# Performance work log

Measured on AMD Instinct MI355X. Metric: run time of the kernel, lower is better.

The kernel has to match this reference:

```python
import jax, jax.numpy as jnp
import numpy as np
from jax import lax

# Key identity used: modulating ALL weights of output channel o by s_o (with no bias
# inside the modulated conv, as in the source where F.conv2d(..., bias=None)) is
# mathematically identical to a plain conv followed by per-(batch, out_channel)
# scaling of the output. This collapses the per-sample Python loop into one conv.

def _upsample2x(x):
    # nearest-neighbor x2, matching F.interpolate(scale_factor=2) default mode
    return jnp.repeat(jnp.repeat(x, 2, axis=2), 2, axis=3)

def _conv(x, w):
    return lax.conv_general_dilated(
        x, w, window_strides=(1, 1), padding=[(1, 1), (1, 1)],
        dimension_numbers=("NCHW", "OIHW", "NCHW"))

def _modconv(x, style, w, fc_w, fc_b):
    # style_fc: [B, style_dim] -> [B, out_ch]
    s = style @ fc_w.T + fc_b          # [B, O]
    y = _conv(x, w)                    # [B, O, H, W]
    return y * s[:, :, None, None]


def setup_inputs() -> dict:
    key = jax.random.key(0)
    ks = jax.random.split(key, 16)
    B, SD = 8, 512
    chans = [(512, 256), (256, 128), (128, 64), (64, 64), (64, 64)]
    inp = {
        "x": jax.random.normal(ks[0], (B, 512, 8, 8), jnp.float32),
        "style": jax.random.normal(ks[1], (B, SD), jnp.float32),
    }
    for i, (ci, co) in enumerate(chans, start=1):
        inp[f"w{i}"] = jax.random.normal(ks[2 * i], (co, ci, 3, 3), jnp.float32) * (1.0 / np.sqrt(ci * 9))
        inp[f"fw{i}"] = jax.random.normal(ks[2 * i + 1], (co, SD), jnp.float32) * (1.0 / np.sqrt(SD))
        inp[f"fb{i}"] = jnp.ones((co,), jnp.float32)
    inp["wf"] = jax.random.normal(ks[12], (3, 64, 3, 3), jnp.float32) * (1.0 / np.sqrt(64 * 9))
    inp["bf"] = jnp.zeros((3,), jnp.float32)
    return inp


def reference(x, style, w1, fw1, fb1, w2, fw2, fb2, w3, fw3, fb3,
              w4, fw4, fb4, w5, fw5, fb5, wf, bf):
    x = _upsample2x(x)
    x = jax.nn.relu(_modconv(x, style, w1, fw1, fb1))
    x = _upsample2x(x)
    x = jax.nn.relu(_modconv(x, style, w2, fw2, fb2))
    x = _upsample2x(x)
    x = jax.nn.relu(_modconv(x, style, w3, fw3, fb3))
    x = _upsample2x(x)
    x = jax.nn.relu(_modconv(x, style, w4, fw4, fb4))
    x = _upsample2x(x)
    x = jax.nn.relu(_modconv(x, style, w5, fw5, fb5))
    x = _conv(x, wf) + bf[None, :, None, None]
    return x
```

## Files before the change

kernel.cpp:

```cpp
#include <hip/hip_runtime.h>
#include <hip/hip_bf16.h>
#include <cstddef>

typedef __bf16 bf16x8 __attribute__((ext_vector_type(8)));
typedef float f32x4 __attribute__((ext_vector_type(4)));


__global__ void convert_x_kernel(const float* __restrict__ x, __hip_bfloat16* __restrict__ act0) {
    int t = blockIdx.x * 256 + threadIdx.x;
    int c = t & 511; int rest = t >> 9;
    int w = rest & 7; rest >>= 3; int h = rest & 7; int b = rest >> 3;
    act0[t] = __float2bfloat16(x[((b * 512 + c) * 8 + h) * 8 + w]);
}

__global__ void wtrans_all_kernel(const float* __restrict__ w1, __hip_bfloat16* __restrict__ o1,
                                  const float* __restrict__ w2, __hip_bfloat16* __restrict__ o2,
                                  const float* __restrict__ w3, __hip_bfloat16* __restrict__ o3,
                                  const float* __restrict__ w4, __hip_bfloat16* __restrict__ o4,
                                  const float* __restrict__ w5, __hip_bfloat16* __restrict__ o5,
                                  const float* __restrict__ wf, __hip_bfloat16* __restrict__ of) {
    int t = blockIdx.x * 256 + threadIdx.x;
    if (t >= 1631232) return;
    if (t < 1548288) {
        const float* w; __hip_bfloat16* o; int lgci, lgco;
        if      (t < 1179648) { w = w1; o = o1; lgci = 9; lgco = 8; }
        else if (t < 1474560) { t -= 1179648; w = w2; o = o2; lgci = 8; lgco = 7; }
        else                  { t -= 1474560; w = w3; o = o3; lgci = 7; lgco = 6; }
        int CI = 1 << lgci;
        int ci = t & (CI - 1);
        int co = (t >> lgci) & ((1 << lgco) - 1);
        int tap = t >> (lgci + lgco);
        o[t] = __float2bfloat16(w[((size_t)co * CI + ci) * 9 + tap]);
    } else if (t < 1622016) {
        const float* w; __hip_bfloat16* o;
        if (t < 1585152) { t -= 1548288; w = w4; o = o4; }
        else             { t -= 1585152; w = w5; o = o5; }
        int j  = t & 7;
        int ln = (t >> 3) & 63;
        int ch = (t >> 9) & 1;
        int nt = (t >> 10) & 3;
        int tap = t >> 12;
        int rr = ln & 15, qq = ln >> 4;
        int co = nt * 16 + rr;
        int ci = ch * 32 + qq * 8 + j;
        o[t] = __float2bfloat16(w[((size_t)co * 64 + ci) * 9 + tap]);
    } else {
        int u = t - 1622016;
        int j  = u & 7;
        int ln = (u >> 3) & 63;
        int ch = (u >> 9) & 1;
        int tap = u >> 10;
        int rr = ln & 15, qq = ln >> 4;
        int ci = ch * 32 + qq * 8 + j;
        float v = (rr < 3) ? wf[((size_t)rr * 64 + ci) * 9 + tap] : 0.f;
        of[u] = __float2bfloat16(v);
    }
}

__global__ void style_all_kernel(const float* __restrict__ style,
                                 const float* __restrict__ fw1, const float* __restrict__ fb1,
                                 const float* __restrict__ fw2, const float* __restrict__ fb2,
                                 const float* __restrict__ fw3, const float* __restrict__ fb3,
                                 const float* __restrict__ fw4, const float* __restrict__ fb4,
                                 const float* __restrict__ fw5, const float* __restrict__ fb5,
                                 float* __restrict__ S) {
    int wvid = blockIdx.x * 4 + (threadIdx.x >> 6);
    int lane = threadIdx.x & 63;
    const float* fw; const float* fb; int lg, sOff, local;
    if      (wvid < 2048) { fw = fw1; fb = fb1; lg = 8; sOff = 0;    local = wvid; }
    else if (wvid < 3072) { fw = fw2; fb = fb2; lg = 7; sOff = 2048; local = wvid - 2048; }
    else if (wvid < 3584) { fw = fw3; fb = fb3; lg = 6; sOff = 3072; local = wvid - 3072; }
    else if (wvid < 4096) { fw = fw4; fb = fb4; lg = 6; sOff = 3584; local = wvid - 3584; }
    else                  { fw = fw5; fb = fb5; lg = 6; sOff = 4096; local = wvid - 4096; }
    int b = local >> lg, o = local & ((1 << lg) - 1);
    const float* sb = style + b * 512;
    const float* fwo = fw + (size_t)o * 512;
    float p = 0.f;
    #pragma unroll
    for (int k = lane; k < 512; k += 64) p += sb[k] * fwo[k];
    #pragma unroll
    for (int off = 32; off > 0; off >>= 1) p += __shfl_down(p, off);
    if (lane == 0) S[sOff + local] = p + fb[o];
}

template <int CI, int CO, int HS, int WS>
__launch_bounds__(256)
__global__ void conv_partial_kernel(const __hip_bfloat16* __restrict__ actIn,
                                    const __hip_bfloat16* __restrict__ wtr,
                                    float* __restrict__ Part) {
    constexpr int HO = HS * 2, WO = WS * 2;
    constexpr size_t sliceN = (size_t)8 * HO * WO * CO;
    const int tid = threadIdx.x;
    const int lane = tid & 63, wv = tid >> 6;
    const int r = lane & 15, q = lane >> 4;
    const int pw = WO / 16, ppb = (HO / 16) * pw;
    const int b = blockIdx.x / ppb;
    const int prest = blockIdx.x - b * ppb;
    const int ph = prest / pw, pwi = prest - ph * pw;
    const int oh0 = ph * 16, ow0 = pwi * 16;
    const int sh0 = oh0 >> 1, sw0 = ow0 >> 1;
    const int n0 = blockIdx.y * 64;
    const int ciOff = blockIdx.z * 64;

    __shared__ alignas(16) __hip_bfloat16 Tile[100 * 72];
    __shared__ alignas(16) __hip_bfloat16 Wlds[2][64 * 72];

    f32x4 acc[4][4];
    #pragma unroll
    for (int i = 0; i < 4; ++i)
        #pragma unroll
        for (int j = 0; j < 4; ++j) acc[i][j] = f32x4{0.f, 0.f, 0.f, 0.f};

    for (int i = tid; i < 800; i += 256) {
        int pix = i >> 3, koct = i & 7;
        int tr = pix / 10, tc2 = pix - tr * 10;
        int su = sh0 - 1 + tr, sv = sw0 - 1 + tc2;
        uint4 v = {0, 0, 0, 0};
        if (su >= 0 && su < HS && sv >= 0 && sv < WS)
            v = *(const uint4*)(actIn + ((size_t)((b * HS + su) * WS + sv) * CI + ciOff + koct * 8));
        *(uint4*)&Tile[pix * 72 + koct * 8] = v;
    }
    for (int i = tid; i < 512; i += 256) {
        int co = i >> 3, koct = i & 7;
        *(uint4*)&Wlds[0][co * 72 + koct * 8] =
            *(const uint4*)(wtr + ((size_t)(n0 + co)) * CI + ciOff + koct * 8);
    }
    __syncthreads();

    #pragma unroll 1
    for (int tap = 0; tap < 9; ++tap) {
        const bool pf = (tap < 8);
        uint4 wr0 = {0,0,0,0}, wr1 = {0,0,0,0};
        if (pf) {
            int co0 = tid >> 3, k0 = tid & 7;
            wr0 = *(const uint4*)(wtr + ((size_t)(tap + 1) * CO + n0 + co0) * CI + ciOff + k0 * 8);
            int i1 = tid + 256; int co1 = i1 >> 3, k1 = i1 & 7;
            wr1 = *(const uint4*)(wtr + ((size_t)(tap + 1) * CO + n0 + co1) * CI + ciOff + k1 * 8);
        }
        const int dyv = tap / 3;
        const int dxm1 = tap - dyv * 3 - 1;
        const int tc = ((r + dxm1) >> 1) + 1;
        int apix[4];
        #pragma unroll
        for (int mt = 0; mt < 4; ++mt)
            apix[mt] = ((((wv * 4 + mt) + dyv - 1) >> 1) + 1) * 10 + tc;

        const int buf = tap & 1;
        #pragma unroll
        for (int ch = 0; ch < 2; ++ch) {
            bf16x8 af[4], bfr[4];
            #pragma unroll
            for (int mt = 0; mt < 4; ++mt)
                af[mt] = *(const bf16x8*)&Tile[apix[mt] * 72 + ch * 32 + q * 8];
            #pragma unroll
            for (int nt = 0; nt < 4; ++nt)
                bfr[nt] = *(const bf16x8*)&Wlds[buf][(nt * 16 + r) * 72 + ch * 32 + q * 8];
            #pragma unroll
            for (int mt = 0; mt < 4; ++mt)
                #pragma unroll
                for (int nt = 0; nt < 4; ++nt)
                    acc[mt][nt] = __builtin_amdgcn_mfma_f32_16x16x32_bf16(
                        af[mt], bfr[nt], acc[mt][nt], 0, 0, 0);
        }
        if (pf) {
            int nb = buf ^ 1;
            { int co0 = tid >> 3, k0 = tid & 7;
              *(uint4*)&Wlds[nb][co0 * 72 + k0 * 8] = wr0; }
            { int i1 = tid + 256; int co1 = i1 >> 3, k1 = i1 & 7;
              *(uint4*)&Wlds[nb][co1 * 72 + k1 * 8] = wr1; }
            __syncthreads();
        }
    }

    float* P = Part + (size_t)blockIdx.z * sliceN;
    #pragma unroll
    for (int mt = 0; mt < 4; ++mt) {
        const int prow = wv * 4 + mt;
        #pragma unroll
        for (int t2 = 0; t2 < 4; ++t2) {
            const int pcol = q * 4 + t2;
            const size_t obase = ((size_t)(b * HO + oh0 + prow) * WO + ow0 + pcol) * CO + n0;
            #pragma unroll
            for (int nt = 0; nt < 4; ++nt)
                P[obase + nt * 16 + r] = acc[mt][nt][t2];
        }
    }
}

template <int KS, int CO, int HW>
__launch_bounds__(256)
__global__ void reduce_kernel(const float* __restrict__ Part, const float* __restrict__ S,
                              __hip_bfloat16* __restrict__ actOut) {
    constexpr size_t sliceN = (size_t)8 * HW * CO;
    size_t e = ((size_t)blockIdx.x * 256 + threadIdx.x) * 4;
    if (e >= sliceN) return;
    f32x4 sum = {0.f, 0.f, 0.f, 0.f};
    #pragma unroll
    for (int k = 0; k < KS; ++k) sum += *(const f32x4*)(Part + (size_t)k * sliceN + e);
    const int co = (int)(e & (CO - 1));
    const int b = (int)(e / ((size_t)HW * CO));
    const float* Sb = S + b * CO + co;
    union { ushort4 u; __hip_bfloat16 h[4]; } pack;
    #pragma unroll
    for (int j = 0; j < 4; ++j)
        pack.h[j] = __float2bfloat16(fmaxf(sum[j] * Sb[j], 0.f));
    *(ushort4*)((unsigned short*)actOut + e) = pack.u;
}

template <int HS, int WS>
__launch_bounds__(256)
__global__ void conv_patch_kernel(const __hip_bfloat16* __restrict__ actIn,
                                  const __hip_bfloat16* __restrict__ wpk,
                                  const float* __restrict__ S,
                                  __hip_bfloat16* __restrict__ actOut) {
    constexpr int HO = HS * 2, WO = WS * 2;

    const int tid = threadIdx.x;
    const int lane = tid & 63, wv = tid >> 6;
    const int r = lane & 15, q = lane >> 4;
    const int lane8 = lane * 8;

    const int pw = WO / 16, ppb = (HO / 16) * pw;
    const int b = blockIdx.x / ppb;
    const int prest = blockIdx.x - b * ppb;
    const int ph = prest / pw, pwi = prest - ph * pw;
    const int oh0 = ph * 16, ow0 = pwi * 16;
    const int sh0 = oh0 >> 1, sw0 = ow0 >> 1;

    __shared__ alignas(16) __hip_bfloat16 Tile[100 * 72];

    f32x4 acc[4][4];
    #pragma unroll
    for (int i = 0; i < 4; ++i)
        #pragma unroll
        for (int j = 0; j < 4; ++j) acc[i][j] = f32x4{0.f, 0.f, 0.f, 0.f};

    const int wv4 = wv * 4;

    for (int i = tid; i < 800; i += 256) {
        int pix = i >> 3, koct = i & 7;
        int tr = pix / 10, tc2 = pix - tr * 10;
        int su = sh0 - 1 + tr, sv = sw0 - 1 + tc2;
        uint4 v = {0, 0, 0, 0};
        if (su >= 0 && su < HS && sv >= 0 && sv < WS)
            v = *(const uint4*)(actIn + ((size_t)((b * HS + su) * WS + sv) * 64 + koct * 8));
        *(uint4*)&Tile[pix * 72 + koct * 8] = v;
    }
    __syncthreads();

    bf16x8 bA[4][2], bB[4][2];

    auto loadB = [&](bf16x8 (&dst)[4][2], int tap) {
        #pragma unroll
        for (int nt = 0; nt < 4; ++nt)
            #pragma unroll
            for (int ch = 0; ch < 2; ++ch)
                dst[nt][ch] = *(const bf16x8*)(wpk + ((tap * 8 + nt * 2 + ch) << 9) + lane8);
    };

    auto compute = [&](int tap, bf16x8 (&bfr)[4][2]) {
        const int dyv = tap / 3;
        const int dxm1 = tap - dyv * 3 - 1;
        const int tc = ((r + dxm1) >> 1) + 1;
        int apix[4];
        #pragma unroll
        for (int mt = 0; mt < 4; ++mt)
            apix[mt] = ((((wv4 + mt) + dyv - 1) >> 1) + 1) * 10 + tc;
        #pragma unroll
        for (int ch = 0; ch < 2; ++ch) {
            bf16x8 af[4];
            #pragma unroll
            for (int mt = 0; mt < 4; ++mt)
                af[mt] = *(const bf16x8*)&Tile[apix[mt] * 72 + ch * 32 + q * 8];
            #pragma unroll
            for (int mt = 0; mt < 4; ++mt)
                #pragma unroll
                for (int nt = 0; nt < 4; ++nt)
                    acc[mt][nt] = __builtin_amdgcn_mfma_f32_16x16x32_bf16(
                        af[mt], bfr[nt][ch], acc[mt][nt], 0, 0, 0);
        }
    };

    loadB(bA, 0);
    #pragma unroll 1
    for (int it = 0; it < 4; ++it) {
        loadB(bB, 2 * it + 1);
        compute(2 * it, bA);
        loadB(bA, 2 * it + 2);
        compute(2 * it + 1, bB);
    }
    compute(8, bA);

    float sv_[4];
    #pragma unroll
    for (int nt = 0; nt < 4; ++nt) sv_[nt] = S[b * 64 + nt * 16 + r];
    #pragma unroll
    for (int mt = 0; mt < 4; ++mt) {
        const int prow = wv4 + mt;
        #pragma unroll
        for (int t2 = 0; t2 < 4; ++t2) {
            const int pcol = q * 4 + t2;
            const size_t obase = ((size_t)(b * HO + oh0 + prow) * WO + ow0 + pcol) * 64;
            #pragma unroll
            for (int nt = 0; nt < 4; ++nt)
                actOut[obase + nt * 16 + r] =
                    __float2bfloat16(fmaxf(acc[mt][nt][t2] * sv_[nt], 0.f));
        }
    }
}

__launch_bounds__(256)
__global__ void conv_final_kernel(const __hip_bfloat16* __restrict__ actIn,
                                  const __hip_bfloat16* __restrict__ wpkF,
                                  const float* __restrict__ bias,
                                  float* __restrict__ out) {
    constexpr int HO = 256, WO = 256;
    const int tid = threadIdx.x, lane = tid & 63, wv = tid >> 6;
    const int r = lane & 15, q = lane >> 4;
    const int lane8 = lane * 8;

    const int ppb = 32 * 16;
    const int b = blockIdx.x / ppb;
    const int prest = blockIdx.x - b * ppb;
    const int ph = prest >> 4, pwi = prest & 15;
    const int oh0 = ph * 8, ow0 = pwi * 16;

    __shared__ alignas(16) __hip_bfloat16 Tile[10 * 18 * 72];

    for (int i = tid; i < 1440; i += 256) {
        int pix = i >> 3, koct = i & 7;
        int tr = pix / 18, tc2 = pix - tr * 18;
        int u = oh0 - 1 + tr, v = ow0 - 1 + tc2;
        uint4 val = {0, 0, 0, 0};
        if (u >= 0 && u < HO && v >= 0 && v < WO)
            val = *(const uint4*)(actIn + ((size_t)((b * HO + u) * WO + v) * 64 + koct * 8));
        *(uint4*)&Tile[pix * 72 + koct * 8] = val;
    }
    __syncthreads();

    f32x4 acc[2];
    acc[0] = f32x4{0.f, 0.f, 0.f, 0.f};
    acc[1] = f32x4{0.f, 0.f, 0.f, 0.f};

    #pragma unroll 1
    for (int tap = 0; tap < 9; ++tap) {
        const int dyv = tap / 3;
        const int dxv = tap - dyv * 3;
        const int tc = r + dxv;
        int apix[2];
        #pragma unroll
        for (int mt = 0; mt < 2; ++mt)
            apix[mt] = (wv * 2 + mt + dyv) * 18 + tc;
        #pragma unroll
        for (int ch = 0; ch < 2; ++ch) {
            bf16x8 bfr = *(const bf16x8*)(wpkF + ((tap * 2 + ch) << 9) + lane8);
            #pragma unroll
            for (int mt = 0; mt < 2; ++mt) {
                bf16x8 af = *(const bf16x8*)&Tile[apix[mt] * 72 + ch * 32 + q * 8];
                acc[mt] = __builtin_amdgcn_mfma_f32_16x16x32_bf16(af, bfr, acc[mt], 0, 0, 0);
            }
        }
    }

    if (r < 3) {
        const float bs = bias[r];
        #pragma unroll
        for (int mt = 0; mt < 2; ++mt) {
            const int prow = wv * 2 + mt;
            #pragma unroll
            for (int t2 = 0; t2 < 4; ++t2) {
                const int pcol = q * 4 + t2;
                out[((size_t)(b * 3 + r) << 16) + (oh0 + prow) * 256 + ow0 + pcol] =
                    acc[mt][t2] + bs;
            }
        }
    }
}

extern "C" void kernel_launch(void* const* d_in, const int* in_sizes, int n_in,
                              void* d_out, int out_size, void* d_ws, size_t ws_size,
                              hipStream_t stream) {
    const float* x    = (const float*)d_in[0];
    const float* sty  = (const float*)d_in[1];
    const float* w1   = (const float*)d_in[2];
    const float* fw1  = (const float*)d_in[3];
    const float* fb1  = (const float*)d_in[4];
    const float* w2   = (const float*)d_in[5];
    const float* fw2  = (const float*)d_in[6];
    const float* fb2  = (const float*)d_in[7];
    const float* w3   = (const float*)d_in[8];
    const float* fw3  = (const float*)d_in[9];
    const float* fb3  = (const float*)d_in[10];
    const float* w4   = (const float*)d_in[11];
    const float* fw4  = (const float*)d_in[12];
    const float* fb4  = (const float*)d_in[13];
    const float* w5   = (const float*)d_in[14];
    const float* fw5  = (const float*)d_in[15];
    const float* fb5  = (const float*)d_in[16];
    const float* wf   = (const float*)d_in[17];
    const float* bf   = (const float*)d_in[18];
    float* out = (float*)d_out;

    char* ws = (char*)d_ws;
    size_t off = 0;
    auto alloc = [&](size_t bytes) {
        char* p = ws + off;
        off += (bytes + 255) & ~(size_t)255;
        return p;
    };
    float* S1 = (float*)alloc(8 * 256 * 4);
    float* S2 = (float*)alloc(8 * 128 * 4);
    float* S3 = (float*)alloc(8 * 64 * 4);
    float* S4 = (float*)alloc(8 * 64 * 4);
    float* S5 = (float*)alloc(8 * 64 * 4);
    __hip_bfloat16* act0 = (__hip_bfloat16*)alloc((size_t)262144 * 2);
    __hip_bfloat16* act1 = (__hip_bfloat16*)alloc((size_t)524288 * 2);
    __hip_bfloat16* act2 = (__hip_bfloat16*)alloc((size_t)1048576 * 2);
    __hip_bfloat16* act3 = (__hip_bfloat16*)alloc((size_t)2097152 * 2);
    __hip_bfloat16* act4 = (__hip_bfloat16*)alloc((size_t)8388608 * 2);
    __hip_bfloat16* act5 = (__hip_bfloat16*)alloc((size_t)33554432 * 2);
    __hip_bfloat16* wt1  = (__hip_bfloat16*)alloc((size_t)9 * 256 * 512 * 2);
    __hip_bfloat16* wt2  = (__hip_bfloat16*)alloc((size_t)9 * 128 * 256 * 2);
    __hip_bfloat16* wt3  = (__hip_bfloat16*)alloc((size_t)9 * 64 * 128 * 2);
    __hip_bfloat16* wt4  = (__hip_bfloat16*)alloc((size_t)9 * 64 * 64 * 2);
    __hip_bfloat16* wt5  = (__hip_bfloat16*)alloc((size_t)9 * 64 * 64 * 2);
    __hip_bfloat16* wtF  = (__hip_bfloat16*)alloc((size_t)9 * 16 * 64 * 2);
    if (off > ws_size) return;

    float* Part = (float*)act5;

    convert_x_kernel<<<1024, 256, 0, stream>>>(x, act0);
    wtrans_all_kernel<<<6372, 256, 0, stream>>>(w1, wt1, w2, wt2, w3, wt3,
                                                w4, wt4, w5, wt5, wf, wtF);
    style_all_kernel<<<1152, 256, 0, stream>>>(sty, fw1, fb1, fw2, fb2, fw3, fb3,
                                               fw4, fb4, fw5, fb5, S1);

    conv_partial_kernel<512, 256, 8, 8><<<dim3(8, 4, 8), 256, 0, stream>>>(act0, wt1, Part);
    reduce_kernel<8, 256, 256><<<512, 256, 0, stream>>>(Part, S1, act1);
    conv_partial_kernel<256, 128, 16, 16><<<dim3(32, 2, 4), 256, 0, stream>>>(act1, wt2, Part);
    reduce_kernel<4, 128, 1024><<<1024, 256, 0, stream>>>(Part, S2, act2);
    conv_partial_kernel<128, 64, 32, 32><<<dim3(128, 1, 2), 256, 0, stream>>>(act2, wt3, Part);
    reduce_kernel<2, 64, 4096><<<2048, 256, 0, stream>>>(Part, S3, act3);

    conv_patch_kernel<64, 64><<<dim3(512), 256, 0, stream>>>(act3, wt4, S4, act4);
    conv_patch_kernel<128, 128><<<dim3(2048), 256, 0, stream>>>(act4, wt5, S5, act5);
    conv_final_kernel<<<4096, 256, 0, stream>>>(act5, wtF, bf, out);
}
```

Before: 228.4 us.

## Use 32x32x16 MFMA in patch conv and 512-thread blocks in partial convs

The 64-channel patch conv kernels now use 32x32x16 bf16 MFMA with a 2x2 accumulator tile instead of 16x16x32 with 4x4, and the packed weight layout for layers 4 and 5 is reordered to match the new B-fragment lane mapping. The early split-K partial conv kernels switch from 256 to 512 threads per block, so each wave handles two pixel rows instead of four and the weight staging takes one load per thread. The aim is fewer MFMA issues and fewer LDS fragment reads in the dominant layers, plus more waves to hide latency in the small early layers. In exchange the epilogue uses a more scattered output index pattern, and larger blocks may reduce how many blocks fit per CU.

```diff
diff --git a/kernel.cpp b/kernel.cpp
--- a/kernel.cpp
+++ b/kernel.cpp
@@ -4,6 +4,7 @@
 
 typedef __bf16 bf16x8 __attribute__((ext_vector_type(8)));
 typedef float f32x4 __attribute__((ext_vector_type(4)));
+typedef float f32x16 __attribute__((ext_vector_type(16)));
 
 
 __global__ void convert_x_kernel(const float* __restrict__ x, __hip_bfloat16* __restrict__ act0) {
@@ -37,12 +38,11 @@
         else             { t -= 1585152; w = w5; o = o5; }
         int j  = t & 7;
         int ln = (t >> 3) & 63;
-        int ch = (t >> 9) & 1;
-        int nt = (t >> 10) & 3;
+        int nt = (t >> 9) & 1;
+        int ks = (t >> 10) & 3;
         int tap = t >> 12;
-        int rr = ln & 15, qq = ln >> 4;
-        int co = nt * 16 + rr;
-        int ci = ch * 32 + qq * 8 + j;
+        int co = nt * 32 + (ln & 31);
+        int ci = ks * 16 + (ln >> 5) * 8 + j;
         o[t] = __float2bfloat16(w[((size_t)co * 64 + ci) * 9 + tap]);
     } else {
         int u = t - 1622016;
@@ -84,7 +84,7 @@
 }
 
 template <int CI, int CO, int HS, int WS>
-__launch_bounds__(256)
+__launch_bounds__(512)
 __global__ void conv_partial_kernel(const __hip_bfloat16* __restrict__ actIn,
                                     const __hip_bfloat16* __restrict__ wtr,
                                     float* __restrict__ Part) {
@@ -105,13 +105,13 @@
     __shared__ alignas(16) __hip_bfloat16 Tile[100 * 72];
     __shared__ alignas(16) __hip_bfloat16 Wlds[2][64 * 72];
 
-    f32x4 acc[4][4];
-    #pragma unroll
-    for (int i = 0; i < 4; ++i)
+    f32x4 acc[2][4];
+    #pragma unroll
+    for (int i = 0; i < 2; ++i)
         #pragma unroll
         for (int j = 0; j < 4; ++j) acc[i][j] = f32x4{0.f, 0.f, 0.f, 0.f};
 
-    for (int i = tid; i < 800; i += 256) {
+    for (int i = tid; i < 800; i += 512) {
         int pix = i >> 3, koct = i & 7;
         int tr = pix / 10, tc2 = pix - tr * 10;
         int su = sh0 - 1 + tr, sv = sw0 - 1 + tc2;
@@ -120,8 +120,8 @@
             v = *(const uint4*)(actIn + ((size_t)((b * HS + su) * WS + sv) * CI + ciOff + koct * 8));
         *(uint4*)&Tile[pix * 72 + koct * 8] = v;
     }
-    for (int i = tid; i < 512; i += 256) {
-        int co = i >> 3, koct = i & 7;
+    {
+        int co = tid >> 3, koct = tid & 7;
         *(uint4*)&Wlds[0][co * 72 + koct * 8] =
             *(const uint4*)(wtr + ((size_t)(n0 + co)) * CI + ciOff + koct * 8);
     }
@@ -130,33 +130,31 @@
     #pragma unroll 1
     for (int tap = 0; tap < 9; ++tap) {
         const bool pf = (tap < 8);
-        uint4 wr0 = {0,0,0,0}, wr1 = {0,0,0,0};
+        uint4 wr0 = {0,0,0,0};
         if (pf) {
             int co0 = tid >> 3, k0 = tid & 7;
             wr0 = *(const uint4*)(wtr + ((size_t)(tap + 1) * CO + n0 + co0) * CI + ciOff + k0 * 8);
-            int i1 = tid + 256; int co1 = i1 >> 3, k1 = i1 & 7;
-            wr1 = *(const uint4*)(wtr + ((size_t)(tap + 1) * CO + n0 + co1) * CI + ciOff + k1 * 8);
         }
         const int dyv = tap / 3;
         const int dxm1 = tap - dyv * 3 - 1;
         const int tc = ((r + dxm1) >> 1) + 1;
-        int apix[4];
-        #pragma unroll
-        for (int mt = 0; mt < 4; ++mt)
-            apix[mt] = ((((wv * 4 + mt) + dyv - 1) >> 1) + 1) * 10 + tc;
+        int apix[2];
+        #pragma unroll
+        for (int mt = 0; mt < 2; ++mt)
+            apix[mt] = ((((wv * 2 + mt) + dyv - 1) >> 1) + 1) * 10 + tc;
 
         const int buf = tap & 1;
         #pragma unroll
         for (int ch = 0; ch < 2; ++ch) {
-            bf16x8 af[4], bfr[4];
-            #pragma unroll
-            for (int mt = 0; mt < 4; ++mt)
+            bf16x8 af[2], bfr[4];
+            #pragma unroll
+            for (int mt = 0; mt < 2; ++mt)
                 af[mt] = *(const bf16x8*)&Tile[apix[mt] * 72 + ch * 32 + q * 8];
             #pragma unroll
             for (int nt = 0; nt < 4; ++nt)
                 bfr[nt] = *(const bf16x8*)&Wlds[buf][(nt * 16 + r) * 72 + ch * 32 + q * 8];
             #pragma unroll
-            for (int mt = 0; mt < 4; ++mt)
+            for (int mt = 0; mt < 2; ++mt)
                 #pragma unroll
                 for (int nt = 0; nt < 4; ++nt)
                     acc[mt][nt] = __builtin_amdgcn_mfma_f32_16x16x32_bf16(
@@ -164,18 +162,16 @@
         }
         if (pf) {
             int nb = buf ^ 1;
-            { int co0 = tid >> 3, k0 = tid & 7;
-              *(uint4*)&Wlds[nb][co0 * 72 + k0 * 8] = wr0; }
-            { int i1 = tid + 256; int co1 = i1 >> 3, k1 = i1 & 7;
-              *(uint4*)&Wlds[nb][co1 * 72 + k1 * 8] = wr1; }
+            int co0 = tid >> 3, k0 = tid & 7;
+            *(uint4*)&Wlds[nb][co0 * 72 + k0 * 8] = wr0;
             __syncthreads();
         }
     }
 
     float* P = Part + (size_t)blockIdx.z * sliceN;
     #pragma unroll
-    for (int mt = 0; mt < 4; ++mt) {
-        const int prow = wv * 4 + mt;
+    for (int mt = 0; mt < 2; ++mt) {
+        const int prow = wv * 2 + mt;
         #pragma unroll
         for (int t2 = 0; t2 < 4; ++t2) {
             const int pcol = q * 4 + t2;
@@ -217,7 +213,10 @@
 
     const int tid = threadIdx.x;
     const int lane = tid & 63, wv = tid >> 6;
-    const int r = lane & 15, q = lane >> 4;
+    const int r32 = lane & 31;
+    const int ko  = lane >> 5;
+    const int pcol = r32 & 15;
+    const int rsub = r32 >> 4;
     const int lane8 = lane * 8;
 
     const int pw = WO / 16, ppb = (HO / 16) * pw;
@@ -229,11 +228,13 @@
 
     __shared__ alignas(16) __hip_bfloat16 Tile[100 * 72];
 
-    f32x4 acc[4][4];
-    #pragma unroll
-    for (int i = 0; i < 4; ++i)
-        #pragma unroll
-        for (int j = 0; j < 4; ++j) acc[i][j] = f32x4{0.f, 0.f, 0.f, 0.f};
+    f32x16 acc[2][2];
+    #pragma unroll
+    for (int i = 0; i < 2; ++i)
+        #pragma unroll
+        for (int j = 0; j < 2; ++j)
+            #pragma unroll
+            for (int k = 0; k < 16; ++k) acc[i][j][k] = 0.f;
 
     const int wv4 = wv * 4;
 
@@ -252,32 +253,34 @@
 
     auto loadB = [&](bf16x8 (&dst)[4][2], int tap) {
         #pragma unroll
-        for (int nt = 0; nt < 4; ++nt)
-            #pragma unroll
-            for (int ch = 0; ch < 2; ++ch)
-                dst[nt][ch] = *(const bf16x8*)(wpk + ((tap * 8 + nt * 2 + ch) << 9) + lane8);
+        for (int ks = 0; ks < 4; ++ks)
+            #pragma unroll
+            for (int nt = 0; nt < 2; ++nt)
+                dst[ks][nt] = *(const bf16x8*)(wpk + (((tap * 4 + ks) * 2 + nt) << 9) + lane8);
     };
 
     auto compute = [&](int tap, bf16x8 (&bfr)[4][2]) {
         const int dyv = tap / 3;
         const int dxm1 = tap - dyv * 3 - 1;
-        const int tc = ((r + dxm1) >> 1) + 1;
-        int apix[4];
-        #pragma unroll
-        for (int mt = 0; mt < 4; ++mt)
-            apix[mt] = ((((wv4 + mt) + dyv - 1) >> 1) + 1) * 10 + tc;
-        #pragma unroll
-        for (int ch = 0; ch < 2; ++ch) {
-            bf16x8 af[4];
-            #pragma unroll
-            for (int mt = 0; mt < 4; ++mt)
-                af[mt] = *(const bf16x8*)&Tile[apix[mt] * 72 + ch * 32 + q * 8];
-            #pragma unroll
-            for (int mt = 0; mt < 4; ++mt)
+        const int tc = ((pcol + dxm1) >> 1) + 1;
+        int apix[2];
+        #pragma unroll
+        for (int mt = 0; mt < 2; ++mt) {
+            const int prow = wv4 + mt * 2 + rsub;
+            apix[mt] = (((prow + dyv - 1) >> 1) + 1) * 10 + tc;
+        }
+        #pragma unroll
+        for (int ks = 0; ks < 4; ++ks) {
+            bf16x8 af[2];
+            #pragma unroll
+            for (int mt = 0; mt < 2; ++mt)
+                af[mt] = *(const bf16x8*)&Tile[apix[mt] * 72 + ks * 16 + ko * 8];
+            #pragma unroll
+            for (int mt = 0; mt < 2; ++mt)
                 #pragma unroll
-                for (int nt = 0; nt < 4; ++nt)
-                    acc[mt][nt] = __builtin_amdgcn_mfma_f32_16x16x32_bf16(
-                        af[mt], bfr[nt][ch], acc[mt][nt], 0, 0, 0);
+                for (int nt = 0; nt < 2; ++nt)
+                    acc[mt][nt] = __builtin_amdgcn_mfma_f32_32x32x16_bf16(
+                        af[mt], bfr[ks][nt], acc[mt][nt], 0, 0, 0);
         }
     };
 
@@ -291,20 +294,22 @@
     }
     compute(8, bA);
 
-    float sv_[4];
-    #pragma unroll
-    for (int nt = 0; nt < 4; ++nt) sv_[nt] = S[b * 64 + nt * 16 + r];
-    #pragma unroll
-    for (int mt = 0; mt < 4; ++mt) {
-        const int prow = wv4 + mt;
-        #pragma unroll
-        for (int t2 = 0; t2 < 4; ++t2) {
-            const int pcol = q * 4 + t2;
-            const size_t obase = ((size_t)(b * HO + oh0 + prow) * WO + ow0 + pcol) * 64;
-            #pragma unroll
-            for (int nt = 0; nt < 4; ++nt)
-                actOut[obase + nt * 16 + r] =
-                    __float2bfloat16(fmaxf(acc[mt][nt][t2] * sv_[nt], 0.f));
+    float sv_[2];
+    #pragma unroll
+    for (int nt = 0; nt < 2; ++nt) sv_[nt] = S[b * 64 + nt * 32 + r32];
+    #pragma unroll
+    for (int mt = 0; mt < 2; ++mt) {
+        #pragma unroll
+        for (int nt = 0; nt < 2; ++nt) {
+            const int co = nt * 32 + r32;
+            #pragma unroll
+            for (int reg = 0; reg < 16; ++reg) {
+                const int m = (reg & 3) + 8 * (reg >> 2) + 4 * ko;
+                const int prow = wv4 + mt * 2 + (m >> 4);
+                const int pc = m & 15;
+                actOut[((size_t)(b * HO + oh0 + prow) * WO + ow0 + pc) * 64 + co] =
+                    __float2bfloat16(fmaxf(acc[mt][nt][reg] * sv_[nt], 0.f));
+            }
         }
     }
 }
@@ -435,11 +440,11 @@
     style_all_kernel<<<1152, 256, 0, stream>>>(sty, fw1, fb1, fw2, fb2, fw3, fb3,
                                                fw4, fb4, fw5, fb5, S1);
 
-    conv_partial_kernel<512, 256, 8, 8><<<dim3(8, 4, 8), 256, 0, stream>>>(act0, wt1, Part);
+    conv_partial_kernel<512, 256, 8, 8><<<dim3(8, 4, 8), 512, 0, stream>>>(act0, wt1, Part);
     reduce_kernel<8, 256, 256><<<512, 256, 0, stream>>>(Part, S1, act1);
-    conv_partial_kernel<256, 128, 16, 16><<<dim3(32, 2, 4), 256, 0, stream>>>(act1, wt2, Part);
+    conv_partial_kernel<256, 128, 16, 16><<<dim3(32, 2, 4), 512, 0, stream>>>(act1, wt2, Part);
     reduce_kernel<4, 128, 1024><<<1024, 256, 0, stream>>>(Part, S2, act2);
-    conv_partial_kernel<128, 64, 32, 32><<<dim3(128, 1, 2), 256, 0, stream>>>(act2, wt3, Part);
+    conv_partial_kernel<128, 64, 32, 32><<<dim3(128, 1, 2), 512, 0, stream>>>(act2, wt3, Part);
     reduce_kernel<2, 64, 4096><<<2048, 256, 0, stream>>>(Part, S3, act3);
 
     conv_patch_kernel<64, 64><<<dim3(512), 256, 0, stream>>>(act3, wt4, S4, act4);
```

Measured after the change: 231.0 us. Within noise of the previous version (+1.1%).
